# Kernel tuning notes

Measured on AMD Instinct MI355X. Metric: run time of the kernel, lower is better.

Reference implementation:

```python
import jax, jax.numpy as jnp
import numpy as np

# static config
B, L, D = 2, 4096, 1024
H, G, WIN = 16, 2, 256
HD = D // H            # 64
KV = G * HD            # 128 (k/v proj width)
E, HID, TOPK = 8, 1024, 2
ENT_W, MAX_USE, EPS = 0.05, 0.4, 1e-8


def setup_inputs() -> dict:
    key = jax.random.key(0)
    ks = jax.random.split(key, 16)
    s = 0.02
    return {
        "x": jax.random.normal(ks[0], (B, L, D), jnp.float32),
        "Wq": jax.random.normal(ks[1], (D, D), jnp.float32) * s,
        "bq": jnp.zeros((D,), jnp.float32),
        "Wk": jax.random.normal(ks[2], (D, KV), jnp.float32) * s,
        "bk": jnp.zeros((KV,), jnp.float32),
        "Wv": jax.random.normal(ks[3], (D, KV), jnp.float32) * s,
        "bv": jnp.zeros((KV,), jnp.float32),
        "Wo": jax.random.normal(ks[4], (D, D), jnp.float32) * s,
        "bo": jnp.zeros((D,), jnp.float32),
        "ln1_g": jnp.ones((D,), jnp.float32),
        "ln1_b": jnp.zeros((D,), jnp.float32),
        "ln2_g": jnp.ones((D,), jnp.float32),
        "ln2_b": jnp.zeros((D,), jnp.float32),
        "Wg": jax.random.normal(ks[5], (D, E), jnp.float32) * 0.01,
        "bg": jnp.zeros((E,), jnp.float32),
        "We": jax.random.normal(ks[6], (E, D, HID), jnp.float32) * s,
        "be": jnp.zeros((E, HID), jnp.float32),
    }


def _layernorm(x, g, b):
    mu = jnp.mean(x, axis=-1, keepdims=True)
    var = jnp.var(x, axis=-1, keepdims=True)
    return (x - mu) * jax.lax.rsqrt(var + 1e-5) * g + b


def _local_attn(x, Wq, bq, Wk, bk, Wv, bv, Wo, bo):
    # overlapping sliding-window bidirectional GQA attention (dropout off / eval)
    Bx, Lx, _ = x.shape
    pad = (-Lx) % WIN
    xp = jnp.pad(x, ((0, 0), (0, pad), (0, 0)))
    Lp = Lx + pad
    q = (xp @ Wq + bq).reshape(Bx, Lp, H, HD).transpose(0, 2, 1, 3)   # [B,H,Lp,hd]
    k = (xp @ Wk + bk).reshape(Bx, Lp, G, HD).transpose(0, 2, 1, 3)   # [B,G,Lp,hd]
    v = (xp @ Wv + bv).reshape(Bx, Lp, G, HD).transpose(0, 2, 1, 3)
    stride = WIN // 2
    nw = (Lp - WIN) // stride + 1
    win_idx = (np.arange(nw)[:, None] * stride + np.arange(WIN)[None, :])
    qw = q[:, :, win_idx]
    kw = k[:, :, win_idx]
    vw = v[:, :, win_idx]
    rep = H // G
    # torch .repeat tiles kv groups: head h uses group h % G, i.e. h = r*G + g
    qw = qw.reshape(Bx, rep, G, nw, WIN, HD)
    scores = jnp.einsum('brgnqd,bgnkd->brgnqk', qw, kw) / np.sqrt(HD)
    attn = jax.nn.softmax(scores, axis=-1)
    o = jnp.einsum('brgnqk,bgnkd->brgnqd', attn, vw)
    o = o.reshape(Bx, H, nw, WIN, HD).transpose(0, 2, 3, 1, 4).reshape(Bx, nw * WIN, D)
    o = o[:, :Lx]                             # truncate concatenated windows to L
    return o @ Wo + bo


def _moe(x, Wg, bg, We, be):
    Bx, Lx, _ = x.shape
    xf = x.reshape(-1, D)                     # [N,D]
    N = xf.shape[0]
    probs = jax.nn.softmax(xf @ Wg + bg, axis=-1)          # [N,E]
    entropy = -jnp.sum(probs * jnp.log(probs + EPS), axis=-1).mean()
    ent_loss = ENT_W * entropy
    topk_p, topk_i = jax.lax.top_k(probs, TOPK)            # [N,K]
    # dense grouped-GEMM reference for top-k dispatch/combine
    all_out = jnp.einsum('nd,edh->neh', xf, We) + be       # [N,E,HID]
    wts = jnp.zeros((N, E), xf.dtype).at[jnp.arange(N)[:, None], topk_i].add(topk_p)
    out = jnp.einsum('ne,neh->nh', wts, all_out)           # [N,HID]
    counts = jnp.zeros((E,), xf.dtype).at[topk_i.reshape(-1)].add(1.0)
    usage = counts / (N + EPS)
    penalty = jnp.sum(jax.nn.relu(usage - MAX_USE))
    return out.reshape(Bx, Lx, HID), ent_loss + penalty


def reference(x, Wq, bq, Wk, bk, Wv, bv, Wo, bo, ln1_g, ln1_b, ln2_g, ln2_b, Wg, bg, We, be):
    h = x + _local_attn(_layernorm(x, ln1_g, ln1_b), Wq, bq, Wk, bk, Wv, bv, Wo, bo)
    moe_out, aux = _moe(_layernorm(h, ln2_g, ln2_b), Wg, bg, We, be)
    out = h + moe_out
    return out, aux
```

## Files before the change

### kernel.cpp

```cpp
#include <hip/hip_runtime.h>
#include <hip/hip_bf16.h>
#include <stdint.h>

typedef __attribute__((ext_vector_type(8))) short bf16x8;
typedef __attribute__((ext_vector_type(8))) _Float16 f16x8;
typedef __attribute__((ext_vector_type(4))) _Float16 f16x4;
typedef __attribute__((ext_vector_type(4))) float f32x4;

__device__ __forceinline__ short f2bf(float f) {
  __hip_bfloat16 h = __float2bfloat16(f);
  union { __hip_bfloat16 h; short s; } u; u.h = h; return u.s;
}

__device__ __forceinline__ unsigned pk2(float a, float b) {
  union { _Float16 h; unsigned short s; } ua, ub;
  ua.h = (_Float16)a; ub.h = (_Float16)b;
  return (unsigned)ua.s | ((unsigned)ub.s << 16);
}

__device__ __forceinline__ void gld16(const void* g, void* l) {
  __builtin_amdgcn_global_load_lds((const __attribute__((address_space(1))) void*)g,
                                   (__attribute__((address_space(3))) void*)l, 16, 0, 0);
}

__device__ __forceinline__ float wave_sum64(float v) {
  #pragma unroll
  for (int off = 1; off < 64; off <<= 1) v += __shfl_xor(v, off);
  return v;
}
__device__ __forceinline__ double wave_sum64d(double v) {
  #pragma unroll
  for (int off = 1; off < 64; off <<= 1) v += __shfl_xor(v, off);
  return v;
}

__global__ __launch_bounds__(256) void ln_split(const float* __restrict__ x,
    const float* __restrict__ g, const float* __restrict__ b,
    _Float16* __restrict__ xh, _Float16* __restrict__ xl) {
  int t = blockIdx.x, tid = threadIdx.x;
  const float4 v = ((const float4*)(x + (size_t)t * 1024))[tid];
  float s = v.x + v.y + v.z + v.w;
  float s2 = v.x*v.x + v.y*v.y + v.z*v.z + v.w*v.w;
  s = wave_sum64(s); s2 = wave_sum64(s2);
  __shared__ float pa[4], pb[4];
  int wid = tid >> 6, lane = tid & 63;
  if (lane == 0) { pa[wid] = s; pb[wid] = s2; }
  __syncthreads();
  float S = pa[0]+pa[1]+pa[2]+pa[3], S2 = pb[0]+pb[1]+pb[2]+pb[3];
  float mu = S * (1.f/1024.f);
  float var = S2 * (1.f/1024.f) - mu*mu;
  float rs = rsqrtf(var + 1e-5f);
  const float4 gv = ((const float4*)g)[tid];
  const float4 bv = ((const float4*)b)[tid];
  float4 o;
  o.x = (v.x-mu)*rs*gv.x + bv.x; o.y = (v.y-mu)*rs*gv.y + bv.y;
  o.z = (v.z-mu)*rs*gv.z + bv.z; o.w = (v.w-mu)*rs*gv.w + bv.w;
  f16x4 hv, lv;
  hv.x = (_Float16)o.x; lv.x = (_Float16)((o.x - (float)hv.x)*2048.f);
  hv.y = (_Float16)o.y; lv.y = (_Float16)((o.y - (float)hv.y)*2048.f);
  hv.z = (_Float16)o.z; lv.z = (_Float16)((o.z - (float)hv.z)*2048.f);
  hv.w = (_Float16)o.w; lv.w = (_Float16)((o.w - (float)hv.w)*2048.f);
  *(f16x4*)&xh[(size_t)t*1024 + tid*4] = hv;
  *(f16x4*)&xl[(size_t)t*1024 + tid*4] = lv;
}

__global__ __launch_bounds__(256) void ln_bf16(const float* __restrict__ x,
    const float* __restrict__ g, const float* __restrict__ b, short* __restrict__ out,
    float2* __restrict__ murs) {
  int t = blockIdx.x, tid = threadIdx.x;
  const float4 v = ((const float4*)(x + (size_t)t * 1024))[tid];
  float s = v.x + v.y + v.z + v.w;
  float s2 = v.x*v.x + v.y*v.y + v.z*v.z + v.w*v.w;
  s = wave_sum64(s); s2 = wave_sum64(s2);
  __shared__ float pa[4], pb[4];
  int wid = tid >> 6, lane = tid & 63;
  if (lane == 0) { pa[wid] = s; pb[wid] = s2; }
  __syncthreads();
  float S = pa[0]+pa[1]+pa[2]+pa[3], S2 = pb[0]+pb[1]+pb[2]+pb[3];
  float mu = S * (1.f/1024.f);
  float var = S2 * (1.f/1024.f) - mu*mu;
  float rs = rsqrtf(var + 1e-5f);
  if (tid == 0) murs[t] = make_float2(mu, rs);
  const float4 gv = ((const float4*)g)[tid];
  const float4 bv = ((const float4*)b)[tid];
  short4 o;
  o.x = f2bf((v.x-mu)*rs*gv.x + bv.x); o.y = f2bf((v.y-mu)*rs*gv.y + bv.y);
  o.z = f2bf((v.z-mu)*rs*gv.z + bv.z); o.w = f2bf((v.w-mu)*rs*gv.w + bv.w);
  ((short4*)(out + (size_t)t * 1024))[tid] = o;
}

__global__ void t_w_f16(const float* __restrict__ src, int srcN,
                        _Float16* __restrict__ dh, _Float16* __restrict__ dl, int dstRow0) {
  __shared__ float tile[32][33];
  int kt = blockIdx.x, nt = blockIdx.y;
  int tx = threadIdx.x, ty = threadIdx.y;
  #pragma unroll
  for (int i = 0; i < 4; i++)
    tile[ty + 8*i][tx] = src[(size_t)(kt*32 + ty + 8*i)*srcN + nt*32 + tx];
  __syncthreads();
  #pragma unroll
  for (int i = 0; i < 4; i++) {
    float v = tile[tx][ty + 8*i];
    _Float16 h = (_Float16)v;
    _Float16 l = (_Float16)((v - (float)h) * 2048.0f);
    size_t o = (size_t)(dstRow0 + nt*32 + ty + 8*i)*1024 + kt*32 + tx;
    dh[o] = h; dl[o] = l;
  }
}

template<int MODE>
__global__ __launch_bounds__(256) void gemm_dma(
    const _Float16* __restrict__ Agh, const _Float16* __restrict__ Agl,
    const _Float16* __restrict__ BTh, const _Float16* __restrict__ BTl,
    const float* __restrict__ b0, const float* __restrict__ b1, const float* __restrict__ b2,
    const float* __restrict__ resid,
    float* __restrict__ out0, float* __restrict__ out1, float* __restrict__ out2) {
  int m0 = blockIdx.x * 128;
  int y = blockIdx.y;
  int n0 = y * 128;
  float* dst; const float* biasp; int dcol0, ld;
  if (MODE == 0) {
    if (y < 8)      { dst = out0; biasp = b0 + y*128; dcol0 = y*128; ld = 1024; }
    else if (y == 8){ dst = out1; biasp = b1; dcol0 = 0; ld = 128; }
    else            { dst = out2; biasp = b2; dcol0 = 0; ld = 128; }
  } else            { dst = out0; biasp = b0 + y*128; dcol0 = y*128; ld = 1024; }

  __shared__ _Float16 AhS[8192];
  __shared__ _Float16 AlS[8192];
  __shared__ _Float16 BhS[8192];
  __shared__ _Float16 BlS[8192];
  int tid = threadIdx.x;
  int lane = tid & 63, w = tid >> 6;
  int wm = (w & 1) * 64, wn = (w >> 1) * 64;
  int l15 = lane & 15, quad = lane >> 4;

  f32x4 accM[4][4] = {};
  f32x4 accC[4][4] = {};

  for (int kb = 0; kb < 1024; kb += 64) {
    __syncthreads();
    #pragma unroll
    for (int i = 0; i < 4; i++) {
      int P = (i*4 + w)*64 + lane;
      int row = P >> 3;
      int c = (P & 7) ^ (row & 7);
      size_t goA = (size_t)(m0 + row)*1024 + kb + c*8;
      size_t goB = (size_t)(n0 + row)*1024 + kb + c*8;
      gld16(Agh + goA, &AhS[P*8]);
      gld16(Agl + goA, &AlS[P*8]);
      gld16(BTh + goB, &BhS[P*8]);
      gld16(BTl + goB, &BlS[P*8]);
    }
    __syncthreads();
    #pragma unroll
    for (int ks = 0; ks < 2; ks++) {
      f16x8 bh[4], bl[4];
      #pragma unroll
      for (int nt = 0; nt < 4; nt++) {
        int row = wn + nt*16 + l15;
        int pc = (ks*4 + quad) ^ (row & 7);
        bh[nt] = *(const f16x8*)&BhS[row*64 + pc*8];
        bl[nt] = *(const f16x8*)&BlS[row*64 + pc*8];
      }
      #pragma unroll
      for (int mt = 0; mt < 4; mt++) {
        int row = wm + mt*16 + l15;
        int pc = (ks*4 + quad) ^ (row & 7);
        f16x8 ah = *(const f16x8*)&AhS[row*64 + pc*8];
        f16x8 al = *(const f16x8*)&AlS[row*64 + pc*8];
        #pragma unroll
        for (int nt = 0; nt < 4; nt++) {
          accM[mt][nt] = __builtin_amdgcn_mfma_f32_16x16x32_f16(ah, bh[nt], accM[mt][nt], 0, 0, 0);
          accC[mt][nt] = __builtin_amdgcn_mfma_f32_16x16x32_f16(ah, bl[nt], accC[mt][nt], 0, 0, 0);
          accC[mt][nt] = __builtin_amdgcn_mfma_f32_16x16x32_f16(al, bh[nt], accC[mt][nt], 0, 0, 0);
        }
      }
    }
  }
  const float inv2048 = 1.0f / 2048.0f;
  #pragma unroll
  for (int mt = 0; mt < 4; mt++)
    #pragma unroll
    for (int r = 0; r < 4; r++) {
      int row = m0 + wm + mt*16 + quad*4 + r;
      #pragma unroll
      for (int nt = 0; nt < 4; nt++) {
        int c = wn + nt*16 + l15;
        float v = accM[mt][nt][r] + accC[mt][nt][r]*inv2048 + biasp[c];
        if (MODE == 1) v += resid[(size_t)row*1024 + dcol0 + c];
        dst[(size_t)row*ld + dcol0 + c] = v;
      }
    }
}

__global__ __launch_bounds__(256, 2) void attn_mfma(
    const float* __restrict__ Qs, const float* __restrict__ Kf, const float* __restrict__ Vf,
    _Float16* __restrict__ Oh, _Float16* __restrict__ Ol) {
  int qb = blockIdx.x, n = blockIdx.y;
  int b = blockIdx.z >> 4, h = blockIdx.z & 15;
  int g = h & 1;
  int tid = threadIdx.x;
  int lane = tid & 63, w = tid >> 6;
  int l15 = lane & 15, quad = lane >> 4;

  __shared__ __align__(16) char smem[70912];
  _Float16* Vt = (_Float16*)smem;
  _Float16* Qh = (_Float16*)(smem + 33792);
  _Float16* Ql = (_Float16*)(smem + 43008);
  _Float16* Kh = (_Float16*)(smem + 52224);
  _Float16* Kl = (_Float16*)(smem + 61440);
  _Float16* Pm = (_Float16*)(smem + 33792);
  float*   linv = (float*)(smem + 70656);

  int qtok0 = b*4096 + n*128 + qb*64;
  int key0  = b*4096 + n*128;

  #pragma unroll
  for (int i = 0; i < 4; i++) {
    int idx = tid + 256*i;
    int row = idx >> 4, c4 = idx & 15;
    float4 v = *(const float4*)&Qs[(size_t)(qtok0+row)*1024 + h*64 + c4*4];
    f16x4 hv, lv;
    hv.x = (_Float16)v.x; lv.x = (_Float16)(v.x - (float)hv.x);
    hv.y = (_Float16)v.y; lv.y = (_Float16)(v.y - (float)hv.y);
    hv.z = (_Float16)v.z; lv.z = (_Float16)(v.z - (float)hv.z);
    hv.w = (_Float16)v.w; lv.w = (_Float16)(v.w - (float)hv.w);
    *(f16x4*)&Qh[row*72 + c4*4] = hv;
    *(f16x4*)&Ql[row*72 + c4*4] = lv;
  }
  {
    int kk = tid >> 4, dd = tid & 15;
    #pragma unroll
    for (int i = 0; i < 8; i++) {
      int p = i*16 + kk;
      float4 v0 = *(const float4*)&Vf[(size_t)(key0 + 2*p    )*128 + g*64 + dd*4];
      float4 v1 = *(const float4*)&Vf[(size_t)(key0 + 2*p + 1)*128 + g*64 + dd*4];
      *(unsigned*)&Vt[(dd*4+0)*264 + 2*p] = pk2(v0.x, v1.x);
      *(unsigned*)&Vt[(dd*4+1)*264 + 2*p] = pk2(v0.y, v1.y);
      *(unsigned*)&Vt[(dd*4+2)*264 + 2*p] = pk2(v0.z, v1.z);
      *(unsigned*)&Vt[(dd*4+3)*264 + 2*p] = pk2(v0.w, v1.w);
    }
  }
  __syncthreads();

  f16x8 qh[2], ql[2];
  {
    int qrow = (w*16 + l15)*72;
    qh[0] = *(const f16x8*)&Qh[qrow + quad*8];
    qh[1] = *(const f16x8*)&Qh[qrow + 32 + quad*8];
    ql[0] = *(const f16x8*)&Ql[qrow + quad*8];
    ql[1] = *(const f16x8*)&Ql[qrow + 32 + quad*8];
  }

  f32x4 S[16];
  #pragma unroll
  for (int t = 0; t < 16; t++) S[t] = (f32x4){0.f,0.f,0.f,0.f};

  for (int c = 0; c < 4; c++) {
    if (c) __syncthreads();
    #pragma unroll
    for (int i = 0; i < 4; i++) {
      int idx = tid + 256*i;
      int row = idx >> 4, c4 = idx & 15;
      float4 v = *(const float4*)&Kf[(size_t)(key0 + c*64 + row)*128 + g*64 + c4*4];
      f16x4 hv, lv;
      hv.x = (_Float16)v.x; lv.x = (_Float16)(v.x - (float)hv.x);
      hv.y = (_Float16)v.y; lv.y = (_Float16)(v.y - (float)hv.y);
      hv.z = (_Float16)v.z; lv.z = (_Float16)(v.z - (float)hv.z);
      hv.w = (_Float16)v.w; lv.w = (_Float16)(v.w - (float)hv.w);
      *(f16x4*)&Kh[row*72 + c4*4] = hv;
      *(f16x4*)&Kl[row*72 + c4*4] = lv;
    }
    __syncthreads();
    #pragma unroll
    for (int t = 0; t < 4; t++) {
      int krow = (t*16 + l15)*72;
      f16x8 kh0 = *(const f16x8*)&Kh[krow + quad*8];
      f16x8 kh1 = *(const f16x8*)&Kh[krow + 32 + quad*8];
      f16x8 kl0 = *(const f16x8*)&Kl[krow + quad*8];
      f16x8 kl1 = *(const f16x8*)&Kl[krow + 32 + quad*8];
      int ti = c*4 + t;
      S[ti] = __builtin_amdgcn_mfma_f32_16x16x32_f16(qh[0], kh0, S[ti], 0, 0, 0);
      S[ti] = __builtin_amdgcn_mfma_f32_16x16x32_f16(ql[0], kh0, S[ti], 0, 0, 0);
      S[ti] = __builtin_amdgcn_mfma_f32_16x16x32_f16(qh[0], kl0, S[ti], 0, 0, 0);
      S[ti] = __builtin_amdgcn_mfma_f32_16x16x32_f16(qh[1], kh1, S[ti], 0, 0, 0);
      S[ti] = __builtin_amdgcn_mfma_f32_16x16x32_f16(ql[1], kh1, S[ti], 0, 0, 0);
      S[ti] = __builtin_amdgcn_mfma_f32_16x16x32_f16(qh[1], kl1, S[ti], 0, 0, 0);
    }
  }

  float lrow[4];
  #pragma unroll
  for (int r = 0; r < 4; r++) {
    float mx = S[0][r];
    #pragma unroll
    for (int t = 1; t < 16; t++) mx = fmaxf(mx, S[t][r]);
    mx = fmaxf(mx, __shfl_xor(mx, 1)); mx = fmaxf(mx, __shfl_xor(mx, 2));
    mx = fmaxf(mx, __shfl_xor(mx, 4)); mx = fmaxf(mx, __shfl_xor(mx, 8));
    float sum = 0.f;
    #pragma unroll
    for (int t = 0; t < 16; t++) {
      float e = __expf((S[t][r] - mx) * 0.125f);
      S[t][r] = e; sum += e;
    }
    sum += __shfl_xor(sum, 1); sum += __shfl_xor(sum, 2);
    sum += __shfl_xor(sum, 4); sum += __shfl_xor(sum, 8);
    lrow[r] = sum;
  }
  if (l15 == 0) {
    #pragma unroll
    for (int r = 0; r < 4; r++) linv[w*16 + quad*4 + r] = 1.f / lrow[r];
  }
  __syncthreads();

  #pragma unroll
  for (int r = 0; r < 4; r++) {
    int q = w*16 + quad*4 + r;
    bool mine = (l15 & 1) ? (r >= 2) : (r < 2);
    #pragma unroll
    for (int t = 0; t < 16; t++) {
      float own = S[t][r];
      float oth = __shfl_xor(own, 1);
      if (mine) {
        float e0 = (l15 & 1) ? oth : own;
        float e1 = (l15 & 1) ? own : oth;
        *(unsigned*)&Pm[q*264 + t*16 + (l15 & ~1)] = pk2(e0, e1);
      }
    }
  }
  __syncthreads();

  f32x4 O[4];
  #pragma unroll
  for (int t = 0; t < 4; t++) O[t] = (f32x4){0.f,0.f,0.f,0.f};
  {
    int prow = (w*16 + l15)*264;
    #pragma unroll
    for (int ks = 0; ks < 8; ks++) {
      f16x8 pa = *(const f16x8*)&Pm[prow + ks*32 + quad*8];
      #pragma unroll
      for (int t = 0; t < 4; t++) {
        f16x8 vb = *(const f16x8*)&Vt[(t*16 + l15)*264 + ks*32 + quad*8];
        O[t] = __builtin_amdgcn_mfma_f32_16x16x32_f16(pa, vb, O[t], 0, 0, 0);
      }
    }
  }

  #pragma unroll
  for (int r = 0; r < 4; r++) {
    int qlocal = w*16 + quad*4 + r;
    float inv = linv[qlocal];
    int orow = b*4096 + n*256 + qb*64 + qlocal;
    #pragma unroll
    for (int t = 0; t < 4; t++) {
      float o = O[t][r] * inv;
      _Float16 oh = (_Float16)o;
      _Float16 ol = (_Float16)((o - (float)oh) * 2048.f);
      size_t oo = (size_t)orow*1024 + h*64 + t*16 + l15;
      Oh[oo] = oh; Ol[oo] = ol;
    }
  }
}

__global__ __launch_bounds__(256) void gating_logits(
    const float* __restrict__ h, const float2* __restrict__ murs,
    const float* __restrict__ g2, const float* __restrict__ b2,
    const float* __restrict__ Wg, const float* __restrict__ bg,
    int* __restrict__ e1e2, float2* __restrict__ p12, float* __restrict__ entArr) {
  int tid = threadIdx.x, lane = tid & 63, wid = tid >> 6;
  int tok = blockIdx.x*4 + wid;
  const float* row = h + (size_t)tok * 1024;
  float2 mr = murs[tok];
  double mu = (double)mr.x, rs = (double)mr.y;
  double acc[8] = {};
  #pragma unroll
  for (int q = 0; q < 4; q++) {
    float4 xv = ((const float4*)row)[lane*4 + q];
    float4 gv = ((const float4*)g2)[lane*4 + q];
    float4 bv = ((const float4*)b2)[lane*4 + q];
    float xs[4] = {xv.x, xv.y, xv.z, xv.w};
    float gs[4] = {gv.x, gv.y, gv.z, gv.w};
    float bs[4] = {bv.x, bv.y, bv.z, bv.w};
    #pragma unroll
    for (int j = 0; j < 4; j++) {
      int i = lane*16 + q*4 + j;
      double xn = ((double)xs[j] - mu) * rs * (double)gs[j] + (double)bs[j];
      const float4 w0 = *(const float4*)&Wg[(size_t)i*8];
      const float4 w1 = *(const float4*)&Wg[(size_t)i*8 + 4];
      acc[0] += xn*(double)w0.x; acc[1] += xn*(double)w0.y;
      acc[2] += xn*(double)w0.z; acc[3] += xn*(double)w0.w;
      acc[4] += xn*(double)w1.x; acc[5] += xn*(double)w1.y;
      acc[6] += xn*(double)w1.z; acc[7] += xn*(double)w1.w;
    }
  }
  #pragma unroll
  for (int e = 0; e < 8; e++) acc[e] = wave_sum64d(acc[e]) + (double)bg[e];
  int e1 = 0;
  #pragma unroll
  for (int e = 1; e < 8; e++) if (acc[e] > acc[e1]) e1 = e;
  int e2 = (e1 == 0) ? 1 : 0;
  #pragma unroll
  for (int e = 0; e < 8; e++) if (e != e1 && acc[e] > acc[e2]) e2 = e;
  float lf[8];
  #pragma unroll
  for (int e = 0; e < 8; e++) lf[e] = (float)acc[e];
  float mx = lf[0];
  #pragma unroll
  for (int e = 1; e < 8; e++) mx = fmaxf(mx, lf[e]);
  float ex[8], Z = 0.f;
  #pragma unroll
  for (int e = 0; e < 8; e++) { ex[e] = __expf(lf[e] - mx); Z += ex[e]; }
  float invZ = 1.f / Z, ent = 0.f;
  float p[8];
  #pragma unroll
  for (int e = 0; e < 8; e++) { p[e] = ex[e]*invZ; ent -= p[e]*__logf(p[e] + 1e-8f); }
  if (lane == 0) {
    e1e2[tok] = e1 | (e2 << 8);
    p12[tok]  = make_float2(p[e1], p[e2]);
    entArr[tok] = ent;
  }
}

__global__ __launch_bounds__(128) void scatter_kernel(
    const int* __restrict__ e1e2, const float2* __restrict__ p12,
    int* __restrict__ cnt, int* __restrict__ bucket, float* __restrict__ bucketP,
    int* __restrict__ bucketS) {
  __shared__ int lcnt[8], base[8];
  int tid = threadIdx.x;
  if (tid < 8) lcnt[tid] = 0;
  __syncthreads();
  int tok = blockIdx.x*128 + tid;
  int ee = e1e2[tok];
  int e1 = ee & 255, e2 = ee >> 8;
  float2 p = p12[tok];
  int o1 = atomicAdd(&lcnt[e1], 1);
  int o2 = atomicAdd(&lcnt[e2], 1);
  __syncthreads();
  if (tid < 8) base[tid] = atomicAdd(&cnt[tid], lcnt[tid]);
  __syncthreads();
  int i1 = base[e1] + o1;
  bucket[e1*8192 + i1] = tok; bucketP[e1*8192 + i1] = p.x; bucketS[e1*8192 + i1] = 0;
  int i2 = base[e2] + o2;
  bucket[e2*8192 + i2] = tok; bucketP[e2*8192 + i2] = p.y; bucketS[e2*8192 + i2] = 1;
}

__global__ __launch_bounds__(256) void aux_kernel(const float* __restrict__ entArr,
    const int* __restrict__ cnt, float* __restrict__ auxOut) {
  int tid = threadIdx.x;
  float s = 0.f;
  for (int i = tid; i < 8192; i += 256) s += entArr[i];
  s = wave_sum64(s);
  __shared__ float pa[4];
  if ((tid & 63) == 0) pa[tid >> 6] = s;
  __syncthreads();
  if (tid == 0) {
    float tot = pa[0]+pa[1]+pa[2]+pa[3];
    float entMean = tot / 8192.f;
    float pen = 0.f;
    for (int e = 0; e < 8; e++) {
      float usage = (float)cnt[e] / (8192.f + 1e-8f);
      pen += fmaxf(usage - 0.4f, 0.f);
    }
    auxOut[0] = 0.05f * entMean + pen;
  }
}

__global__ void transpose_We(const float* __restrict__ We, short* __restrict__ WeT) {
  int e = blockIdx.z;
  __shared__ float tile[32][33];
  int kt = blockIdx.x, nt = blockIdx.y;
  int tx = threadIdx.x, ty = threadIdx.y;
  const float* src = We + (size_t)e * 1048576;
  short* dst = WeT + (size_t)e * 1048576;
  #pragma unroll
  for (int i = 0; i < 4; i++)
    tile[ty + 8*i][tx] = src[(size_t)(kt*32 + ty + 8*i)*1024 + nt*32 + tx];
  __syncthreads();
  #pragma unroll
  for (int i = 0; i < 4; i++)
    dst[(size_t)(nt*32 + ty + 8*i)*1024 + kt*32 + tx] = f2bf(tile[tx][ty + 8*i]);
}

__global__ __launch_bounds__(256) void moe_gemm(
    const short* __restrict__ hln, const short* __restrict__ WeT,
    const float* __restrict__ be, const int* __restrict__ cnt,
    const int* __restrict__ bucket, const float* __restrict__ bucketP,
    const int* __restrict__ bucketS,
    float* __restrict__ slot0, float* __restrict__ slot1) {
  int e = blockIdx.z;
  int count = cnt[e];
  int mtile = blockIdx.x;
  if (mtile * 128 >= count) return;
  int n0 = blockIdx.y * 128;
  __shared__ short As[8192];
  __shared__ short Bs[8192];
  __shared__ int   toks[128];
  __shared__ float pws[128];
  __shared__ int   sls[128];
  int tid = threadIdx.x;
  if (tid < 128) {
    int idx = mtile*128 + tid;
    int ic = idx < count ? idx : count - 1;
    toks[tid] = bucket[e*8192 + ic];
    pws[tid]  = bucketP[e*8192 + ic];
    sls[tid]  = bucketS[e*8192 + ic];
  }
  __syncthreads();
  int lane = tid & 63, w = tid >> 6;
  int wm = (w & 1) * 64, wn = (w >> 1) * 64;
  int l15 = lane & 15, quad = lane >> 4;
  const short* Bt = WeT + (size_t)e * 1048576;

  size_t goA[4], goB[4];
  int Pc[4];
  #pragma unroll
  for (int i = 0; i < 4; i++) {
    int P = (i*4 + w)*64 + lane;
    int row = P >> 3;
    int c = (P & 7) ^ (row & 7);
    Pc[i] = P;
    goA[i] = (size_t)toks[row]*1024 + c*8;
    goB[i] = (size_t)(n0 + row)*1024 + c*8;
  }

  f32x4 acc[4][4] = {};
  for (int kb = 0; kb < 1024; kb += 64) {
    __syncthreads();
    #pragma unroll
    for (int i = 0; i < 4; i++) {
      gld16(hln + goA[i] + kb, &As[Pc[i]*8]);
      gld16(Bt  + goB[i] + kb, &Bs[Pc[i]*8]);
    }
    __syncthreads();
    #pragma unroll
    for (int ks = 0; ks < 2; ks++) {
      bf16x8 af[4], bfr[4];
      #pragma unroll
      for (int nt = 0; nt < 4; nt++) {
        int row = wn + nt*16 + l15;
        int pc = (ks*4 + quad) ^ (row & 7);
        bfr[nt] = *(const bf16x8*)&Bs[row*64 + pc*8];
      }
      #pragma unroll
      for (int mt = 0; mt < 4; mt++) {
        int row = wm + mt*16 + l15;
        int pc = (ks*4 + quad) ^ (row & 7);
        af[mt] = *(const bf16x8*)&As[row*64 + pc*8];
        #pragma unroll
        for (int nt = 0; nt < 4; nt++)
          acc[mt][nt] = __builtin_amdgcn_mfma_f32_16x16x32_bf16(af[mt], bfr[nt], acc[mt][nt], 0, 0, 0);
      }
    }
  }
  #pragma unroll
  for (int mt = 0; mt < 4; mt++) {
    #pragma unroll
    for (int r = 0; r < 4; r++) {
      int m = wm + mt*16 + quad*4 + r;
      if (mtile*128 + m < count) {
        int tok = toks[m];
        float pp = pws[m];
        float* dst = sls[m] ? slot1 : slot0;
        #pragma unroll
        for (int nt = 0; nt < 4; nt++) {
          int col = n0 + wn + nt*16 + l15;
          dst[(size_t)tok*1024 + col] = pp * (acc[mt][nt][r] + be[e*1024 + col]);
        }
      }
    }
  }
}

__global__ __launch_bounds__(256) void final_add(float* __restrict__ out,
    const float* __restrict__ s0, const float* __restrict__ s1) {
  const int total = 8388608 / 4;
  for (int i = blockIdx.x*256 + threadIdx.x; i < total; i += gridDim.x*256) {
    float4 a = ((float4*)out)[i];
    const float4 x0 = ((const float4*)s0)[i];
    const float4 x1 = ((const float4*)s1)[i];
    a.x += x0.x + x1.x; a.y += x0.y + x1.y; a.z += x0.z + x1.z; a.w += x0.w + x1.w;
    ((float4*)out)[i] = a;
  }
}

extern "C" void kernel_launch(void* const* d_in, const int* in_sizes, int n_in,
                              void* d_out, int out_size, void* d_ws, size_t ws_size,
                              hipStream_t stream) {
  const float* x    = (const float*)d_in[0];
  const float* Wq   = (const float*)d_in[1];
  const float* bq   = (const float*)d_in[2];
  const float* Wk   = (const float*)d_in[3];
  const float* bk   = (const float*)d_in[4];
  const float* Wv   = (const float*)d_in[5];
  const float* bv   = (const float*)d_in[6];
  const float* Wo   = (const float*)d_in[7];
  const float* bo   = (const float*)d_in[8];
  const float* ln1g = (const float*)d_in[9];
  const float* ln1b = (const float*)d_in[10];
  const float* ln2g = (const float*)d_in[11];
  const float* ln2b = (const float*)d_in[12];
  const float* Wg   = (const float*)d_in[13];
  const float* bg   = (const float*)d_in[14];
  const float* We   = (const float*)d_in[15];
  const float* be   = (const float*)d_in[16];
  float* out = (float*)d_out;

  char* ws = (char*)d_ws;
  size_t off = 0;
  auto alloc = [&](size_t bytes) { char* p = ws + off; off += (bytes + 255) & ~(size_t)255; return p; };
  _Float16* xh  = (_Float16*)alloc(16777216);
  _Float16* xl  = (_Float16*)alloc(16777216);
  float* Qs    = (float*)alloc(33554432);
  float* Kf    = (float*)alloc(4194304);
  float* Vf    = (float*)alloc(4194304);
  short* WeT   = (short*)alloc(16777216);
  float* slot0 = (float*)alloc(33554432);
  float* slot1 = (float*)alloc(33554432);
  int*   bucket  = (int*)alloc(262144);
  float* bucketP = (float*)alloc(262144);
  int*   bucketS = (int*)alloc(262144);
  int*   cnt     = (int*)alloc(256);
  float* entArr  = (float*)alloc(32768);
  int*   e1e2    = (int*)alloc(32768);
  float2* p12    = (float2*)alloc(65536);
  float2* murs   = (float2*)alloc(65536);
  _Float16* Oh = xh;
  _Float16* Ol = xl;
  short* hln   = (short*)Qs;
  _Float16* WoTh    = (_Float16*)slot0;
  _Float16* WoTl    = (_Float16*)(slot0 + 524288);
  _Float16* BTqkv_h = (_Float16*)slot1;
  _Float16* BTqkv_l = (_Float16*)((char*)slot1 + 2621440);

  hipMemsetAsync(cnt, 0, 256, stream);
  t_w_f16<<<dim3(32, 32), dim3(32, 8), 0, stream>>>(Wq, 1024, BTqkv_h, BTqkv_l, 0);
  t_w_f16<<<dim3(32, 4),  dim3(32, 8), 0, stream>>>(Wk, 128,  BTqkv_h, BTqkv_l, 1024);
  t_w_f16<<<dim3(32, 4),  dim3(32, 8), 0, stream>>>(Wv, 128,  BTqkv_h, BTqkv_l, 1152);
  t_w_f16<<<dim3(32, 32), dim3(32, 8), 0, stream>>>(Wo, 1024, WoTh, WoTl, 0);
  transpose_We<<<dim3(32,32,8), dim3(32,8), 0, stream>>>(We, WeT);

  ln_split<<<8192, 256, 0, stream>>>(x, ln1g, ln1b, xh, xl);
  gemm_dma<0><<<dim3(64,10), 256, 0, stream>>>(xh, xl, BTqkv_h, BTqkv_l, bq, bk, bv,
                                               nullptr, Qs, Kf, Vf);
  attn_mfma<<<dim3(4,16,32), 256, 0, stream>>>(Qs, Kf, Vf, Oh, Ol);
  gemm_dma<1><<<dim3(64,8), 256, 0, stream>>>(Oh, Ol, WoTh, WoTl, bo, nullptr, nullptr,
                                              x, out, nullptr, nullptr);
  ln_bf16<<<8192, 256, 0, stream>>>(out, ln2g, ln2b, hln, murs);
  gating_logits<<<2048, 256, 0, stream>>>(out, murs, ln2g, ln2b, Wg, bg, e1e2, p12, entArr);
  scatter_kernel<<<64, 128, 0, stream>>>(e1e2, p12, cnt, bucket, bucketP, bucketS);
  aux_kernel<<<1, 256, 0, stream>>>(entArr, cnt, out + 8388608);
  moe_gemm<<<dim3(64,8,8), 256, 0, stream>>>(hln, WeT, be, cnt, bucket, bucketP, bucketS, slot0, slot1);
  final_add<<<2048, 256, 0, stream>>>(out, slot0, slot1);
}
```

Baseline: 566.8 us.

## Shrink projection GEMM tile to 64x128 and double-buffer LDS loads

The split-f16 projection GEMM now uses 64-row M tiles and a K step of 32, with two LDS buffers so the next tile's global-to-LDS DMA is issued while the current tile is consumed by MFMAs. The grid doubles to 128 blocks along M and launch bounds request 3 waves per SIMD, both aimed at raising occupancy on the many-CU device. This also cuts the per-K-step sync count to one. In exchange B tiles are reloaded twice as often across blocks, and each K step has fewer MFMAs to hide load latency.

```diff
diff --git a/kernel.cpp b/kernel.cpp
--- a/kernel.cpp
+++ b/kernel.cpp
@@ -109,13 +109,13 @@
 }
 
 template<int MODE>
-__global__ __launch_bounds__(256) void gemm_dma(
+__global__ __launch_bounds__(256, 3) void gemm_dma(
     const _Float16* __restrict__ Agh, const _Float16* __restrict__ Agl,
     const _Float16* __restrict__ BTh, const _Float16* __restrict__ BTl,
     const float* __restrict__ b0, const float* __restrict__ b1, const float* __restrict__ b2,
     const float* __restrict__ resid,
     float* __restrict__ out0, float* __restrict__ out1, float* __restrict__ out2) {
-  int m0 = blockIdx.x * 128;
+  int m0 = blockIdx.x * 64;
   int y = blockIdx.y;
   int n0 = y * 128;
   float* dst; const float* biasp; int dcol0, ld;
@@ -125,61 +125,75 @@
     else            { dst = out2; biasp = b2; dcol0 = 0; ld = 128; }
   } else            { dst = out0; biasp = b0 + y*128; dcol0 = y*128; ld = 1024; }
 
-  __shared__ _Float16 AhS[8192];
-  __shared__ _Float16 AlS[8192];
-  __shared__ _Float16 BhS[8192];
-  __shared__ _Float16 BlS[8192];
+  __shared__ _Float16 AhS[2][2048];
+  __shared__ _Float16 AlS[2][2048];
+  __shared__ _Float16 BhS[2][4096];
+  __shared__ _Float16 BlS[2][4096];
   int tid = threadIdx.x;
   int lane = tid & 63, w = tid >> 6;
-  int wm = (w & 1) * 64, wn = (w >> 1) * 64;
+  int wm = (w & 1) * 32, wn = (w >> 1) * 64;
   int l15 = lane & 15, quad = lane >> 4;
 
-  f32x4 accM[4][4] = {};
-  f32x4 accC[4][4] = {};
-
-  for (int kb = 0; kb < 1024; kb += 64) {
-    __syncthreads();
-    #pragma unroll
-    for (int i = 0; i < 4; i++) {
-      int P = (i*4 + w)*64 + lane;
-      int row = P >> 3;
-      int c = (P & 7) ^ (row & 7);
-      size_t goA = (size_t)(m0 + row)*1024 + kb + c*8;
-      size_t goB = (size_t)(n0 + row)*1024 + kb + c*8;
-      gld16(Agh + goA, &AhS[P*8]);
-      gld16(Agl + goA, &AlS[P*8]);
-      gld16(BTh + goB, &BhS[P*8]);
-      gld16(BTl + goB, &BlS[P*8]);
-    }
-    __syncthreads();
-    #pragma unroll
-    for (int ks = 0; ks < 2; ks++) {
-      f16x8 bh[4], bl[4];
+  int Pa = tid;
+  int cA = (Pa & 3) ^ ((Pa >> 4) & 3);
+  size_t gA = (size_t)(m0 + (Pa >> 2)) * 1024 + cA * 8;
+  int Pb0 = tid, Pb1 = tid + 256;
+  int cB0 = (Pb0 & 3) ^ ((Pb0 >> 4) & 3);
+  int cB1 = (Pb1 & 3) ^ ((Pb1 >> 4) & 3);
+  size_t gB0 = (size_t)(n0 + (Pb0 >> 2)) * 1024 + cB0 * 8;
+  size_t gB1 = (size_t)(n0 + (Pb1 >> 2)) * 1024 + cB1 * 8;
+
+  f32x4 accM[2][4] = {};
+  f32x4 accC[2][4] = {};
+
+  gld16(Agh + gA, &AhS[0][Pa*8]);
+  gld16(Agl + gA, &AlS[0][Pa*8]);
+  gld16(BTh + gB0, &BhS[0][Pb0*8]);
+  gld16(BTh + gB1, &BhS[0][Pb1*8]);
+  gld16(BTl + gB0, &BlS[0][Pb0*8]);
+  gld16(BTl + gB1, &BlS[0][Pb1*8]);
+  __syncthreads();
+
+  int cur = 0;
+  for (int it = 0; it < 32; ++it) {
+    if (it < 31) {
+      int kb = (it + 1) * 32;
+      int nb = cur ^ 1;
+      gld16(Agh + gA + kb, &AhS[nb][Pa*8]);
+      gld16(Agl + gA + kb, &AlS[nb][Pa*8]);
+      gld16(BTh + gB0 + kb, &BhS[nb][Pb0*8]);
+      gld16(BTh + gB1 + kb, &BhS[nb][Pb1*8]);
+      gld16(BTl + gB0 + kb, &BlS[nb][Pb0*8]);
+      gld16(BTl + gB1 + kb, &BlS[nb][Pb1*8]);
+    }
+    f16x8 bh[4], bl[4];
+    #pragma unroll
+    for (int nt = 0; nt < 4; nt++) {
+      int row = wn + nt*16 + l15;
+      int pc = quad ^ ((row >> 2) & 3);
+      bh[nt] = *(const f16x8*)&BhS[cur][row*32 + pc*8];
+      bl[nt] = *(const f16x8*)&BlS[cur][row*32 + pc*8];
+    }
+    #pragma unroll
+    for (int mt = 0; mt < 2; mt++) {
+      int row = wm + mt*16 + l15;
+      int pc = quad ^ ((row >> 2) & 3);
+      f16x8 ah = *(const f16x8*)&AhS[cur][row*32 + pc*8];
+      f16x8 al = *(const f16x8*)&AlS[cur][row*32 + pc*8];
       #pragma unroll
       for (int nt = 0; nt < 4; nt++) {
-        int row = wn + nt*16 + l15;
-        int pc = (ks*4 + quad) ^ (row & 7);
-        bh[nt] = *(const f16x8*)&BhS[row*64 + pc*8];
-        bl[nt] = *(const f16x8*)&BlS[row*64 + pc*8];
+        accM[mt][nt] = __builtin_amdgcn_mfma_f32_16x16x32_f16(ah, bh[nt], accM[mt][nt], 0, 0, 0);
+        accC[mt][nt] = __builtin_amdgcn_mfma_f32_16x16x32_f16(ah, bl[nt], accC[mt][nt], 0, 0, 0);
+        accC[mt][nt] = __builtin_amdgcn_mfma_f32_16x16x32_f16(al, bh[nt], accC[mt][nt], 0, 0, 0);
       }
-      #pragma unroll
-      for (int mt = 0; mt < 4; mt++) {
-        int row = wm + mt*16 + l15;
-        int pc = (ks*4 + quad) ^ (row & 7);
-        f16x8 ah = *(const f16x8*)&AhS[row*64 + pc*8];
-        f16x8 al = *(const f16x8*)&AlS[row*64 + pc*8];
-        #pragma unroll
-        for (int nt = 0; nt < 4; nt++) {
-          accM[mt][nt] = __builtin_amdgcn_mfma_f32_16x16x32_f16(ah, bh[nt], accM[mt][nt], 0, 0, 0);
-          accC[mt][nt] = __builtin_amdgcn_mfma_f32_16x16x32_f16(ah, bl[nt], accC[mt][nt], 0, 0, 0);
-          accC[mt][nt] = __builtin_amdgcn_mfma_f32_16x16x32_f16(al, bh[nt], accC[mt][nt], 0, 0, 0);
-        }
-      }
-    }
-  }
+    }
+    __syncthreads();
+    cur ^= 1;
+  }
+
   const float inv2048 = 1.0f / 2048.0f;
   #pragma unroll
-  for (int mt = 0; mt < 4; mt++)
+  for (int mt = 0; mt < 2; mt++)
     #pragma unroll
     for (int r = 0; r < 4; r++) {
       int row = m0 + wm + mt*16 + quad*4 + r;
@@ -640,11 +654,11 @@
   transpose_We<<<dim3(32,32,8), dim3(32,8), 0, stream>>>(We, WeT);
 
   ln_split<<<8192, 256, 0, stream>>>(x, ln1g, ln1b, xh, xl);
-  gemm_dma<0><<<dim3(64,10), 256, 0, stream>>>(xh, xl, BTqkv_h, BTqkv_l, bq, bk, bv,
-                                               nullptr, Qs, Kf, Vf);
+  gemm_dma<0><<<dim3(128,10), 256, 0, stream>>>(xh, xl, BTqkv_h, BTqkv_l, bq, bk, bv,
+                                                nullptr, Qs, Kf, Vf);
   attn_mfma<<<dim3(4,16,32), 256, 0, stream>>>(Qs, Kf, Vf, Oh, Ol);
-  gemm_dma<1><<<dim3(64,8), 256, 0, stream>>>(Oh, Ol, WoTh, WoTl, bo, nullptr, nullptr,
-                                              x, out, nullptr, nullptr);
+  gemm_dma<1><<<dim3(128,8), 256, 0, stream>>>(Oh, Ol, WoTh, WoTl, bo, nullptr, nullptr,
+                                               x, out, nullptr, nullptr);
   ln_bf16<<<8192, 256, 0, stream>>>(out, ln2g, ln2b, hln, murs);
   gating_logits<<<2048, 256, 0, stream>>>(out, murs, ln2g, ln2b, Wg, bg, e1e2, p12, entArr);
   scatter_kernel<<<64, 128, 0, stream>>>(e1e2, p12, cnt, bucket, bucketP, bucketS);
```

After: 564.0 us. About the same (-0.5%).
